# Optimization experiments

Hardware: AMD Instinct MI355X
Metric: run time of the kernel (lower is better)

## Reference

```python
import jax, jax.numpy as jnp
import numpy as np

N_NODES = 50000
N_FEAT = 32
HIDDEN = 64
K_HOPS = 3
N_EDGES = 800000
BN_EPS = 1e-5


def setup_inputs() -> dict:
    key = jax.random.key(0)
    ks = jax.random.split(key, 16)
    x = jax.random.normal(ks[0], (N_NODES, N_FEAT), jnp.float32)
    edge_index = jax.random.randint(ks[1], (2, N_EDGES), 0, N_NODES, jnp.int32)
    edge_weight = jax.random.uniform(ks[2], (N_EDGES,), jnp.float32, minval=0.1, maxval=1.0)
    fin = N_FEAT + HIDDEN  # DCRNN cell concatenates [X, H]
    s = 1.0 / np.sqrt(fin)
    Wz = jax.random.uniform(ks[3], (2, K_HOPS, fin, HIDDEN), jnp.float32, -s, s)
    Wr = jax.random.uniform(ks[4], (2, K_HOPS, fin, HIDDEN), jnp.float32, -s, s)
    Wh = jax.random.uniform(ks[5], (2, K_HOPS, fin, HIDDEN), jnp.float32, -s, s)
    bz = jax.random.uniform(ks[6], (HIDDEN,), jnp.float32, -s, s)
    br = jax.random.uniform(ks[7], (HIDDEN,), jnp.float32, -s, s)
    bh = jax.random.uniform(ks[8], (HIDDEN,), jnp.float32, -s, s)
    g = 1.0 / np.sqrt(HIDDEN)
    gcn_w = jax.random.uniform(ks[9], (HIDDEN, HIDDEN), jnp.float32, -g, g)
    gcn_b = jax.random.uniform(ks[10], (HIDDEN,), jnp.float32, -g, g)
    bn_gamma = jnp.ones((HIDDEN,), jnp.float32)
    bn_beta = jnp.zeros((HIDDEN,), jnp.float32)
    lin_w = jax.random.uniform(ks[11], (HIDDEN, 1), jnp.float32, -g, g)
    lin_b = jax.random.uniform(ks[12], (1,), jnp.float32, -g, g)
    return dict(x=x, edge_index=edge_index, edge_weight=edge_weight,
                Wz=Wz, bz=bz, Wr=Wr, br=br, Wh=Wh, bh=bh,
                gcn_w=gcn_w, gcn_b=gcn_b, bn_gamma=bn_gamma, bn_beta=bn_beta,
                lin_w=lin_w, lin_b=lin_b)


def _dconv(X, W, b, row, col, ew, do_inv, di_inv, n):
    # Diffusion conv: H = sum_k T_out^k(X) @ W[0,k] + T_in^k(X) @ W[1,k] + b
    # T_out: propagate along edges (source -> target), out-degree normalized
    # T_in : propagate along reversed edges, in-degree normalized
    H = X @ W[0, 0] + X @ W[1, 0]
    Tx_o = X
    Tx_i = X
    w_out = (ew * do_inv[row])[:, None]  # [E,1]
    w_in = (ew * di_inv[col])[:, None]   # [E,1]
    for k in range(1, W.shape[1]):
        Tx_o = jax.ops.segment_sum(w_out * Tx_o[row], col, num_segments=n)
        Tx_i = jax.ops.segment_sum(w_in * Tx_i[col], row, num_segments=n)
        H = H + Tx_o @ W[0, k] + Tx_i @ W[1, k]
    return H + b


def reference(x, edge_index, edge_weight, Wz, bz, Wr, br, Wh, bh,
              gcn_w, gcn_b, bn_gamma, bn_beta, lin_w, lin_b):
    n = x.shape[0]
    row, col = edge_index[0], edge_index[1]
    # weighted degrees (as in DConv's dense-adjacency degree computation)
    deg_out = jax.ops.segment_sum(edge_weight, row, num_segments=n)
    deg_in = jax.ops.segment_sum(edge_weight, col, num_segments=n)
    do_inv = jnp.where(deg_out > 0, 1.0 / deg_out, 0.0)
    di_inv = jnp.where(deg_in > 0, 1.0 / deg_in, 0.0)

    # --- DCRNN cell (GRU with diffusion convs), hidden state starts at zero ---
    H0 = jnp.zeros((n, Wz.shape[-1]), x.dtype)
    XH = jnp.concatenate([x, H0], axis=1)
    Z = jax.nn.sigmoid(_dconv(XH, Wz, bz, row, col, edge_weight, do_inv, di_inv, n))
    R = jax.nn.sigmoid(_dconv(XH, Wr, br, row, col, edge_weight, do_inv, di_inv, n))
    XHR = jnp.concatenate([x, H0 * R], axis=1)
    H_tilde = jnp.tanh(_dconv(XHR, Wh, bh, row, col, edge_weight, do_inv, di_inv, n))
    H = Z * H0 + (1.0 - Z) * H_tilde  # [N, HIDDEN]

    # --- GCNConv(H, edge_index) with unit edge weights + self loops, sym norm ---
    xw = H @ gcn_w
    ones_e = jnp.ones((row.shape[0],), x.dtype)
    deg = jax.ops.segment_sum(ones_e, col, num_segments=n) + 1.0  # + self loop
    dis = jnp.where(deg > 0, jax.lax.rsqrt(deg), 0.0)
    norm = (dis[row] * dis[col])[:, None]
    y = jax.ops.segment_sum(norm * xw[row], col, num_segments=n) + (dis * dis)[:, None] * xw
    y = y + gcn_b

    # ReLU -> BatchNorm1d (batch statistics, biased var) -> Dropout(identity/eval) -> Linear
    y = jax.nn.relu(y)
    mean = jnp.mean(y, axis=0)
    var = jnp.mean(jnp.square(y - mean), axis=0)
    y = (y - mean) * jax.lax.rsqrt(var + BN_EPS) * bn_gamma + bn_beta
    out = y @ lin_w + lin_b  # [N, 1]
    return out
```

## Files before the change

### kernel.cpp

```cpp
#include <hip/hip_runtime.h>
#include <hip/hip_fp16.h>
#include <math.h>


#define BN_EPS 1e-5f
#define CAPB 6
#define CAP  64
#define ITEMS 2048
#define KI 8
#define REGCAP 5120

typedef _Float16 v8h __attribute__((ext_vector_type(8)));
typedef float v4f __attribute__((ext_vector_type(4)));

__global__ __launch_bounds__(256) void k_sort1(
    const int* __restrict__ row, const int* __restrict__ col,
    const float* __restrict__ ew,
    unsigned long long* __restrict__ bufC, unsigned long long* __restrict__ bufR,
    unsigned* __restrict__ gcnt, int E, int nbk, int reg) {
    __shared__ unsigned hist[256], scanb[256], cur[256], runb[256];
    __shared__ unsigned long long outb[ITEMS];
    int t = threadIdx.x;
    int s = (blockIdx.x >= nbk) ? 1 : 0;
    int blk = blockIdx.x - s * nbk;
    int e0 = blk * ITEMS;
    int vcnt = E - e0; if (vcnt > ITEMS) vcnt = ITEMS;
    hist[t] = 0;
    __syncthreads();
    for (int k = 0; k < KI; ++k) {
        int e = e0 + k * 256 + t;
        if (e < E) {
            int key = s ? row[e] : col[e];
            atomicAdd(&hist[key >> 8], 1u);
        }
    }
    __syncthreads();
    scanb[t] = hist[t];
    __syncthreads();
    for (int off = 1; off < 256; off <<= 1) {
        unsigned v = (t >= off) ? scanb[t - off] : 0u;
        __syncthreads();
        scanb[t] += v;
        __syncthreads();
    }
    unsigned excl = scanb[t] - hist[t];
    __syncthreads();
    scanb[t] = excl;
    cur[t] = excl;
    runb[t] = (unsigned)(t * reg) + atomicAdd(&gcnt[s * 256 + t], hist[t]);
    __syncthreads();
    for (int k = 0; k < KI; ++k) {
        int e = e0 + k * 256 + t;
        if (e < E) {
            int key, oth;
            if (s) { key = row[e]; oth = col[e]; }
            else   { key = col[e]; oth = row[e]; }
            unsigned hw = (unsigned)__half_as_ushort(__float2half(ew[e]));
            unsigned long long it = ((unsigned long long)(unsigned)key << 32)
                                  | ((unsigned)oth << 16) | hw;
            unsigned r = atomicAdd(&cur[key >> 8], 1u);
            outb[r] = it;
        }
    }
    __syncthreads();
    unsigned long long* buf = s ? bufR : bufC;
    for (int k = 0; k < KI; ++k) {
        int idx = k * 256 + t;
        if (idx < vcnt) {
            unsigned long long it = outb[idx];
            unsigned d = (unsigned)(it >> 40) & 255u;
            buf[(size_t)runb[d] + ((unsigned)idx - scanb[d])] = it;
        }
    }
}

__global__ __launch_bounds__(256) void k_sort2(
    const unsigned long long* __restrict__ buf, const unsigned* __restrict__ gcnt,
    unsigned* __restrict__ ent, int* __restrict__ cnt, int N, int reg) {
    __shared__ unsigned hist[256], scanb[256], cur[256];
    __shared__ unsigned outp[REGCAP];
    __shared__ unsigned char outl[REGCAP];
    int t = threadIdx.x;
    int d0 = blockIdx.x;
    const unsigned long long* src = buf + (size_t)d0 * reg;
    int cin = (int)gcnt[d0]; if (cin > REGCAP) cin = REGCAP;
    hist[t] = 0;
    __syncthreads();
    for (int i = t; i < cin; i += 256) {
        unsigned l = (unsigned)(src[i] >> 32) & 255u;
        atomicAdd(&hist[l], 1u);
    }
    __syncthreads();
    scanb[t] = hist[t];
    __syncthreads();
    for (int off = 1; off < 256; off <<= 1) {
        unsigned v = (t >= off) ? scanb[t - off] : 0u;
        __syncthreads();
        scanb[t] += v;
        __syncthreads();
    }
    unsigned excl = scanb[t] - hist[t];
    __syncthreads();
    scanb[t] = excl;
    cur[t] = excl;
    int node0 = d0 << 8;
    if (node0 + t < N) cnt[node0 + t] = (int)hist[t];
    __syncthreads();
    for (int i = t; i < cin; i += 256) {
        unsigned long long it = src[i];
        unsigned l = (unsigned)(it >> 32) & 255u;
        unsigned r = atomicAdd(&cur[l], 1u);
        outp[r] = (unsigned)it;
        outl[r] = (unsigned char)l;
    }
    __syncthreads();
    for (int i = t; i < cin; i += 256) {
        unsigned l = outl[i];
        int slot = i - (int)scanb[l];
        int node = node0 + (int)l;
        if (slot < CAP && node < N)
            ent[((size_t)node << CAPB) + slot] = outp[i];
    }
}

__device__ inline float ent_w(unsigned e) {
    return __half2float(__ushort_as_half((unsigned short)(e & 0xffffu)));
}

__global__ void k_degs(const unsigned* __restrict__ ent_col, const unsigned* __restrict__ ent_row,
                       const int* __restrict__ cnt_col, const int* __restrict__ cnt_row,
                       float* __restrict__ do_inv, float* __restrict__ di_inv,
                       float* __restrict__ dis, int N) {
    int i = blockIdx.x * blockDim.x + threadIdx.x;
    if (i >= N) return;
    float s = 0.f;
    int c = min(cnt_row[i], CAP);
    const unsigned* er = ent_row + ((size_t)i << CAPB);
    for (int j = 0; j < c; ++j) s += ent_w(er[j]);
    do_inv[i] = s > 0.f ? 1.f / s : 0.f;
    s = 0.f;
    c = min(cnt_col[i], CAP);
    const unsigned* ec = ent_col + ((size_t)i << CAPB);
    for (int j = 0; j < c; ++j) s += ent_w(ec[j]);
    di_inv[i] = s > 0.f ? 1.f / s : 0.f;
    dis[i] = rsqrtf((float)cnt_col[i] + 1.0f);
}

__global__ void k_cvt_x(const float* __restrict__ xf, __half* __restrict__ xh, int n2) {
    int t = blockIdx.x * blockDim.x + threadIdx.x;
    if (t >= n2) return;
    float2 v = *(const float2*)(xf + 2 * (size_t)t);
    __half2 h; h.x = __float2half(v.x); h.y = __float2half(v.y);
    *(__half2*)(xh + 2 * (size_t)t) = h;
}

__global__ void k_hop(const unsigned* __restrict__ ent_col, const unsigned* __restrict__ ent_row,
                      const int* __restrict__ cnt_col, const int* __restrict__ cnt_row,
                      const __half* __restrict__ So, const __half* __restrict__ Si,
                      const float* __restrict__ do_inv, const float* __restrict__ di_inv,
                      __half* __restrict__ Do, __half* __restrict__ Di, int N) {
    int t = blockIdx.x * blockDim.x + threadIdx.x;
    int f = t & 31;
    int p = t >> 5;
    if (p >= 2 * N) return;
    const unsigned* ent; const __half* S; const float* inv; __half* D;
    int d, cnt;
    if (p < N) { d = p;     ent = ent_col; S = So; inv = do_inv; D = Do; cnt = min(cnt_col[d], CAP); }
    else       { d = p - N; ent = ent_row; S = Si; inv = di_inv; D = Di; cnt = min(cnt_row[d], CAP); }
    ent += ((size_t)d << CAPB);
    float acc = 0.f;
    int j = 0;
    for (; j + 7 < cnt; j += 8) {
        unsigned e0 = ent[j],     e1 = ent[j + 1], e2 = ent[j + 2], e3 = ent[j + 3];
        unsigned e4 = ent[j + 4], e5 = ent[j + 5], e6 = ent[j + 6], e7 = ent[j + 7];
        int s0 = e0 >> 16, s1 = e1 >> 16, s2 = e2 >> 16, s3 = e3 >> 16;
        int s4 = e4 >> 16, s5 = e5 >> 16, s6 = e6 >> 16, s7 = e7 >> 16;
        float i0 = inv[s0], i1 = inv[s1], i2 = inv[s2], i3 = inv[s3];
        float i4 = inv[s4], i5 = inv[s5], i6 = inv[s6], i7 = inv[s7];
        float v0 = __half2float(S[(size_t)s0 * 32 + f]);
        float v1 = __half2float(S[(size_t)s1 * 32 + f]);
        float v2 = __half2float(S[(size_t)s2 * 32 + f]);
        float v3 = __half2float(S[(size_t)s3 * 32 + f]);
        float v4 = __half2float(S[(size_t)s4 * 32 + f]);
        float v5 = __half2float(S[(size_t)s5 * 32 + f]);
        float v6 = __half2float(S[(size_t)s6 * 32 + f]);
        float v7 = __half2float(S[(size_t)s7 * 32 + f]);
        acc += ent_w(e0) * i0 * v0 + ent_w(e1) * i1 * v1
             + ent_w(e2) * i2 * v2 + ent_w(e3) * i3 * v3
             + ent_w(e4) * i4 * v4 + ent_w(e5) * i5 * v5
             + ent_w(e6) * i6 * v6 + ent_w(e7) * i7 * v7;
    }
    for (; j + 3 < cnt; j += 4) {
        unsigned e0 = ent[j],     e1 = ent[j + 1];
        unsigned e2 = ent[j + 2], e3 = ent[j + 3];
        int s0 = e0 >> 16, s1 = e1 >> 16, s2 = e2 >> 16, s3 = e3 >> 16;
        float i0 = inv[s0], i1 = inv[s1], i2 = inv[s2], i3 = inv[s3];
        float v0 = __half2float(S[(size_t)s0 * 32 + f]);
        float v1 = __half2float(S[(size_t)s1 * 32 + f]);
        float v2 = __half2float(S[(size_t)s2 * 32 + f]);
        float v3 = __half2float(S[(size_t)s3 * 32 + f]);
        acc += ent_w(e0) * i0 * v0 + ent_w(e1) * i1 * v1
             + ent_w(e2) * i2 * v2 + ent_w(e3) * i3 * v3;
    }
    for (; j < cnt; ++j) {
        unsigned e0 = ent[j];
        int s0 = e0 >> 16;
        acc += ent_w(e0) * inv[s0] * __half2float(S[(size_t)s0 * 32 + f]);
    }
    D[(size_t)d * 32 + f] = __float2half(acc);
}

__global__ void k_wprep(const float* __restrict__ Wz, const float* __restrict__ Wh,
                        const float* __restrict__ gcn_w,
                        __half* __restrict__ wzT, __half* __restrict__ whT,
                        __half* __restrict__ gwT) {
    int t = blockIdx.x * blockDim.x + threadIdx.x;
    if (t < 64 * 160) {
        int c = t / 160, k = t % 160;
        int blk = k >> 5, r = k & 31;
        float vz, vh;
        if (blk == 0) {
            vz = Wz[r * 64 + c] + Wz[(288 + r) * 64 + c];
            vh = Wh[r * 64 + c] + Wh[(288 + r) * 64 + c];
        } else {
            int kk = (blk + 1) >> 1, dd = (blk + 1) & 1;
            int off = ((dd * 3 + kk) * 96 + r) * 64 + c;
            vz = Wz[off]; vh = Wh[off];
        }
        wzT[t] = __float2half(vz);
        whT[t] = __float2half(vh);
    }
    if (t < 64 * 64) {
        int c = t >> 6, k = t & 63;
        gwT[t] = __float2half(gcn_w[k * 64 + c]);
    }
}

__device__ inline v8h ldh8(const __half* p) { return *(const v8h*)p; }

__global__ __launch_bounds__(256) void k_zh_mfma(
    const __half* __restrict__ xh, const __half* __restrict__ t1o,
    const __half* __restrict__ t1i, const __half* __restrict__ t2o,
    const __half* __restrict__ t2i,
    const __half* __restrict__ wzT, const __half* __restrict__ whT,
    const float* __restrict__ bz, const float* __restrict__ bh,
    const float* __restrict__ dis, __half* __restrict__ Hd, int N) {
    int lane = threadIdx.x & 63;
    int wv = threadIdx.x >> 6;
    int q = lane >> 4, m = lane & 15;
    int c = wv * 16 + m;
    int ko = q * 8;

    const __half* wz = wzT + c * 160 + ko;
    const __half* wh = whT + c * 160 + ko;
    v8h bz0 = ldh8(wz),       bh0 = ldh8(wh);
    v8h bz1 = ldh8(wz + 32),  bh1 = ldh8(wh + 32);
    v8h bz2 = ldh8(wz + 64),  bh2 = ldh8(wh + 64);
    v8h bz3 = ldh8(wz + 96),  bh3 = ldh8(wh + 96);
    v8h bz4 = ldh8(wz + 128), bh4 = ldh8(wh + 128);
    float bzc = bz[c], bhc = bh[c];

    int T = (N + 15) >> 4;
    for (int t = blockIdx.x; t < T; t += gridDim.x) {
        int n0 = t << 4;
        int nn = n0 + m; if (nn > N - 1) nn = N - 1;
        size_t off = (size_t)nn * 32 + ko;
        v8h a0 = ldh8(xh + off);
        v8h a1 = ldh8(t1o + off);
        v8h a2 = ldh8(t1i + off);
        v8h a3 = ldh8(t2o + off);
        v8h a4 = ldh8(t2i + off);
        v4f az = {0.f, 0.f, 0.f, 0.f}, ah = {0.f, 0.f, 0.f, 0.f};
        az = __builtin_amdgcn_mfma_f32_16x16x32_f16(a0, bz0, az, 0, 0, 0);
        ah = __builtin_amdgcn_mfma_f32_16x16x32_f16(a0, bh0, ah, 0, 0, 0);
        az = __builtin_amdgcn_mfma_f32_16x16x32_f16(a1, bz1, az, 0, 0, 0);
        ah = __builtin_amdgcn_mfma_f32_16x16x32_f16(a1, bh1, ah, 0, 0, 0);
        az = __builtin_amdgcn_mfma_f32_16x16x32_f16(a2, bz2, az, 0, 0, 0);
        ah = __builtin_amdgcn_mfma_f32_16x16x32_f16(a2, bh2, ah, 0, 0, 0);
        az = __builtin_amdgcn_mfma_f32_16x16x32_f16(a3, bz3, az, 0, 0, 0);
        ah = __builtin_amdgcn_mfma_f32_16x16x32_f16(a3, bh3, ah, 0, 0, 0);
        az = __builtin_amdgcn_mfma_f32_16x16x32_f16(a4, bz4, az, 0, 0, 0);
        ah = __builtin_amdgcn_mfma_f32_16x16x32_f16(a4, bh4, ah, 0, 0, 0);

#pragma unroll
        for (int i = 0; i < 4; ++i) {
            float zv = 1.f / (1.f + expf(-(az[i] + bzc)));
            float hv = (1.f - zv) * tanhf(ah[i] + bhc);
            int node = n0 + q * 4 + i;
            if (node < N) Hd[(size_t)node * 64 + c] = __float2half(dis[node] * hv);
        }
    }
}

__global__ __launch_bounds__(256) void k_agg(
    const unsigned* __restrict__ ent_col, const int* __restrict__ cnt_col,
    const float* __restrict__ dis, const __half* __restrict__ Hd,
    float* __restrict__ P, int N) {
    int t = blockIdx.x * blockDim.x + threadIdx.x;
    int ch = t & 63;
    int d = t >> 6;
    if (d >= N) return;
    const unsigned* ent = ent_col + ((size_t)d << CAPB);
    int cnt = min(cnt_col[d], CAP);
    float acc = __half2float(Hd[(size_t)d * 64 + ch]);
    int j = 0;
    for (; j + 7 < cnt; j += 8) {
        unsigned e0 = ent[j],     e1 = ent[j + 1], e2 = ent[j + 2], e3 = ent[j + 3];
        unsigned e4 = ent[j + 4], e5 = ent[j + 5], e6 = ent[j + 6], e7 = ent[j + 7];
        float v0 = __half2float(Hd[(size_t)(e0 >> 16) * 64 + ch]);
        float v1 = __half2float(Hd[(size_t)(e1 >> 16) * 64 + ch]);
        float v2 = __half2float(Hd[(size_t)(e2 >> 16) * 64 + ch]);
        float v3 = __half2float(Hd[(size_t)(e3 >> 16) * 64 + ch]);
        float v4 = __half2float(Hd[(size_t)(e4 >> 16) * 64 + ch]);
        float v5 = __half2float(Hd[(size_t)(e5 >> 16) * 64 + ch]);
        float v6 = __half2float(Hd[(size_t)(e6 >> 16) * 64 + ch]);
        float v7 = __half2float(Hd[(size_t)(e7 >> 16) * 64 + ch]);
        acc += (v0 + v1 + v2 + v3) + (v4 + v5 + v6 + v7);
    }
    for (; j + 3 < cnt; j += 4) {
        unsigned e0 = ent[j],     e1 = ent[j + 1];
        unsigned e2 = ent[j + 2], e3 = ent[j + 3];
        float v0 = __half2float(Hd[(size_t)(e0 >> 16) * 64 + ch]);
        float v1 = __half2float(Hd[(size_t)(e1 >> 16) * 64 + ch]);
        float v2 = __half2float(Hd[(size_t)(e2 >> 16) * 64 + ch]);
        float v3 = __half2float(Hd[(size_t)(e3 >> 16) * 64 + ch]);
        acc += v0 + v1 + v2 + v3;
    }
    for (; j < cnt; ++j) {
        acc += __half2float(Hd[(size_t)(ent[j] >> 16) * 64 + ch]);
    }
    P[(size_t)d * 64 + ch] = dis[d] * acc;
}

__global__ __launch_bounds__(256) void k_gcn2(
    const float* __restrict__ P, const __half* __restrict__ gwT,
    const float* __restrict__ gcn_b,
    float* __restrict__ y, float* __restrict__ stats, int N) {
    __shared__ float red[2][256];
    int lane = threadIdx.x & 63;
    int wv = threadIdx.x >> 6;
    int q = lane >> 4, m = lane & 15;
    int c = wv * 16 + m;
    int ko = q * 8;
    v8h g0 = ldh8(gwT + c * 64 + ko);
    v8h g1 = ldh8(gwT + c * 64 + 32 + ko);
    float bl = gcn_b[c];
    float sa = 0.f, s2a = 0.f;
    int T = (N + 15) >> 4;
    for (int t = blockIdx.x; t < T; t += gridDim.x) {
        int n0 = t << 4;
        int nn = n0 + m; if (nn > N - 1) nn = N - 1;
        const float* pr = P + (size_t)nn * 64;
        v4f p0 = *(const v4f*)(pr + ko);
        v4f p1 = *(const v4f*)(pr + ko + 4);
        v4f p2 = *(const v4f*)(pr + 32 + ko);
        v4f p3 = *(const v4f*)(pr + 32 + ko + 4);
        v8h a0, a1;
#pragma unroll
        for (int j = 0; j < 4; ++j) {
            a0[j] = (_Float16)p0[j]; a0[4 + j] = (_Float16)p1[j];
            a1[j] = (_Float16)p2[j]; a1[4 + j] = (_Float16)p3[j];
        }
        v4f acc = {0.f, 0.f, 0.f, 0.f};
        acc = __builtin_amdgcn_mfma_f32_16x16x32_f16(a0, g0, acc, 0, 0, 0);
        acc = __builtin_amdgcn_mfma_f32_16x16x32_f16(a1, g1, acc, 0, 0, 0);
#pragma unroll
        for (int i = 0; i < 4; ++i) {
            int node = n0 + q * 4 + i;
            if (node < N) {
                float v = acc[i] + bl;
                v = v > 0.f ? v : 0.f;
                y[(size_t)node * 64 + c] = v;
                sa += v; s2a += v * v;
            }
        }
    }
    red[0][threadIdx.x] = sa;
    red[1][threadIdx.x] = s2a;
    __syncthreads();
    if (q == 0) {
        int t0 = threadIdx.x;
        float ts  = red[0][t0] + red[0][t0 + 16] + red[0][t0 + 32] + red[0][t0 + 48];
        float ts2 = red[1][t0] + red[1][t0 + 16] + red[1][t0 + 32] + red[1][t0 + 48];
        atomicAdd(&stats[c], ts);
        atomicAdd(&stats[64 + c], ts2);
    }
}

__global__ void k_final(const float* __restrict__ y, const float* __restrict__ stats,
                        const float* __restrict__ gma, const float* __restrict__ bta,
                        const float* __restrict__ lw, const float* __restrict__ lb,
                        float* __restrict__ out, int N) {
    int lane = threadIdx.x & 63;
    int wave = (blockIdx.x * blockDim.x + threadIdx.x) >> 6;
    if (wave >= N) return;
    float invN = 1.0f / (float)N;
    float mean = stats[lane] * invN;
    float var  = stats[64 + lane] * invN - mean * mean;
    float istd = rsqrtf(var + BN_EPS);
    float v = y[(size_t)wave * 64 + lane];
    float t = (v - mean) * istd * gma[lane] + bta[lane];
    float p = t * lw[lane];
    for (int off = 32; off > 0; off >>= 1)
        p += __shfl_down(p, off, 64);
    if (lane == 0) out[wave] = p + lb[0];
}

extern "C" void kernel_launch(void* const* d_in, const int* in_sizes, int n_in,
                              void* d_out, int out_size, void* d_ws, size_t ws_size,
                              hipStream_t stream) {
    const float* x     = (const float*)d_in[0];
    const int*   ei    = (const int*)d_in[1];
    const float* ew    = (const float*)d_in[2];
    const float* Wz    = (const float*)d_in[3];
    const float* bz    = (const float*)d_in[4];
    const float* Wh    = (const float*)d_in[7];
    const float* bhv   = (const float*)d_in[8];
    const float* gcn_w = (const float*)d_in[9];
    const float* gcn_b = (const float*)d_in[10];
    const float* gma   = (const float*)d_in[11];
    const float* bta   = (const float*)d_in[12];
    const float* lw    = (const float*)d_in[13];
    const float* lb    = (const float*)d_in[14];
    float* out = (float*)d_out;

    const int N = in_sizes[0] / 32;
    const int E = in_sizes[2];
    const int* row = ei;
    const int* col = ei + E;

    float* ws      = (float*)d_ws;
    int*   cnt_col = (int*)ws;
    int*   cnt_row = (int*)(ws + (size_t)N);
    unsigned* gcnt = (unsigned*)(ws + 2 * (size_t)N);
    float* stats   = ws + 2 * (size_t)N + 512;
    size_t Z0      = 2 * (size_t)N + 640;
    float* dis     = ws + Z0;
    float* do_inv  = ws + Z0 + (size_t)N;
    float* di_inv  = ws + Z0 + 2 * (size_t)N;
    __half* xh     = (__half*)(ws + Z0 + 3 * (size_t)N);
    __half* txo1   = (__half*)(ws + Z0 + 19 * (size_t)N);
    __half* txi1   = (__half*)(ws + Z0 + 35 * (size_t)N);
    __half* txo2   = (__half*)(ws + Z0 + 51 * (size_t)N);
    __half* txi2   = (__half*)(ws + Z0 + 67 * (size_t)N);
    unsigned* ent_col = (unsigned*)(ws + Z0 + 83 * (size_t)N);
    unsigned* ent_row = ent_col + ((size_t)N << CAPB);
    __half* wzT    = (__half*)(ws + Z0 + 211 * (size_t)N);
    __half* whT    = wzT + 64 * 160;
    __half* gwT    = whT + 64 * 160;

    unsigned long long* bufC = (unsigned long long*)ent_row;
    unsigned long long* bufR = (unsigned long long*)txo1;
    __half* Hd = (__half*)ent_row;
    float*  P  = (float*)xh;
    float*  yb = (float*)ent_col;

    size_t zero_bytes = (2 * (size_t)N + 640) * sizeof(float);
    hipMemsetAsync(d_ws, 0, zero_bytes, stream);

    int NB = (N + 255) / 256;
    int nbk = (E + ITEMS - 1) / ITEMS;
    int ndig = (N + 255) / 256;
    k_cvt_x<<<(16 * N + 255) / 256, 256, 0, stream>>>(x, xh, 16 * N);
    k_wprep<<<40, 256, 0, stream>>>(Wz, Wh, gcn_w, wzT, whT, gwT);
    k_sort1<<<2 * nbk, 256, 0, stream>>>(row, col, ew, bufC, bufR, gcnt, E, nbk, REGCAP);
    k_sort2<<<ndig, 256, 0, stream>>>(bufC, gcnt,       ent_col, cnt_col, N, REGCAP);
    k_sort2<<<ndig, 256, 0, stream>>>(bufR, gcnt + 256, ent_row, cnt_row, N, REGCAP);
    k_degs <<<NB, 256, 0, stream>>>(ent_col, ent_row, cnt_col, cnt_row,
                                    do_inv, di_inv, dis, N);

    int bhop = (2 * N * 32 + 255) / 256;
    k_hop<<<bhop, 256, 0, stream>>>(ent_col, ent_row, cnt_col, cnt_row,
                                    xh, xh, do_inv, di_inv, txo1, txi1, N);
    k_hop<<<bhop, 256, 0, stream>>>(ent_col, ent_row, cnt_col, cnt_row,
                                    txo1, txi1, do_inv, di_inv, txo2, txi2, N);

    k_zh_mfma<<<1024, 256, 0, stream>>>(xh, txo1, txi1, txo2, txi2,
                                        wzT, whT, bz, bhv, dis, Hd, N);

    k_agg<<<(64 * N + 255) / 256, 256, 0, stream>>>(ent_col, cnt_col, dis, Hd, P, N);
    k_gcn2<<<1024, 256, 0, stream>>>(P, gwT, gcn_b, yb, stats, N);
    k_final<<<(N + 3) / 4, 256, 0, stream>>>(yb, stats, gma, bta, lw, lb, out, N);
}
```

Before: 298.2 us.

## Fuse degree computation into merged sort2 launch and store GCN intermediate in fp16

```diff
diff --git a/kernel.cpp b/kernel.cpp
--- a/kernel.cpp
+++ b/kernel.cpp
@@ -74,16 +74,26 @@
     }
 }
 
+__device__ inline float ent_w(unsigned e) {
+    return __half2float(__ushort_as_half((unsigned short)(e & 0xffffu)));
+}
+
 __global__ __launch_bounds__(256) void k_sort2(
-    const unsigned long long* __restrict__ buf, const unsigned* __restrict__ gcnt,
-    unsigned* __restrict__ ent, int* __restrict__ cnt, int N, int reg) {
+    const unsigned long long* __restrict__ bufC, const unsigned long long* __restrict__ bufR,
+    const unsigned* __restrict__ gcnt,
+    unsigned* __restrict__ ent_col, unsigned* __restrict__ ent_row,
+    int* __restrict__ cnt_col, int* __restrict__ cnt_row,
+    float* __restrict__ di_inv, float* __restrict__ do_inv, float* __restrict__ dis,
+    int N, int reg, int ndig) {
     __shared__ unsigned hist[256], scanb[256], cur[256];
     __shared__ unsigned outp[REGCAP];
     __shared__ unsigned char outl[REGCAP];
     int t = threadIdx.x;
-    int d0 = blockIdx.x;
-    const unsigned long long* src = buf + (size_t)d0 * reg;
-    int cin = (int)gcnt[d0]; if (cin > REGCAP) cin = REGCAP;
+    int s = (blockIdx.x >= ndig) ? 1 : 0;
+    int d0 = blockIdx.x - s * ndig;
+    const unsigned long long* src = (s ? bufR : bufC) + (size_t)d0 * reg;
+    unsigned* ent = s ? ent_row : ent_col;
+    int cin = (int)gcnt[s * 256 + d0]; if (cin > REGCAP) cin = REGCAP;
     hist[t] = 0;
     __syncthreads();
     for (int i = t; i < cin; i += 256) {
@@ -103,8 +113,6 @@
     __syncthreads();
     scanb[t] = excl;
     cur[t] = excl;
-    int node0 = d0 << 8;
-    if (node0 + t < N) cnt[node0 + t] = (int)hist[t];
     __syncthreads();
     for (int i = t; i < cin; i += 256) {
         unsigned long long it = src[i];
@@ -114,6 +122,7 @@
         outl[r] = (unsigned char)l;
     }
     __syncthreads();
+    int node0 = d0 << 8;
     for (int i = t; i < cin; i += 256) {
         unsigned l = outl[i];
         int slot = i - (int)scanb[l];
@@ -121,29 +130,16 @@
         if (slot < CAP && node < N)
             ent[((size_t)node << CAPB) + slot] = outp[i];
     }
-}
-
-__device__ inline float ent_w(unsigned e) {
-    return __half2float(__ushort_as_half((unsigned short)(e & 0xffffu)));
-}
-
-__global__ void k_degs(const unsigned* __restrict__ ent_col, const unsigned* __restrict__ ent_row,
-                       const int* __restrict__ cnt_col, const int* __restrict__ cnt_row,
-                       float* __restrict__ do_inv, float* __restrict__ di_inv,
-                       float* __restrict__ dis, int N) {
-    int i = blockIdx.x * blockDim.x + threadIdx.x;
-    if (i >= N) return;
-    float s = 0.f;
-    int c = min(cnt_row[i], CAP);
-    const unsigned* er = ent_row + ((size_t)i << CAPB);
-    for (int j = 0; j < c; ++j) s += ent_w(er[j]);
-    do_inv[i] = s > 0.f ? 1.f / s : 0.f;
-    s = 0.f;
-    c = min(cnt_col[i], CAP);
-    const unsigned* ec = ent_col + ((size_t)i << CAPB);
-    for (int j = 0; j < c; ++j) s += ent_w(ec[j]);
-    di_inv[i] = s > 0.f ? 1.f / s : 0.f;
-    dis[i] = rsqrtf((float)cnt_col[i] + 1.0f);
+    int node = node0 + t;
+    if (node < N) {
+        unsigned beg = scanb[t], n = hist[t];
+        float sum = 0.f;
+        for (unsigned j = 0; j < n; ++j) sum += ent_w(outp[beg + j]);
+        float inv = sum > 0.f ? 1.f / sum : 0.f;
+        if (s) { do_inv[node] = inv; cnt_row[node] = (int)n; }
+        else   { di_inv[node] = inv; cnt_col[node] = (int)n;
+                 dis[node] = rsqrtf((float)n + 1.0f); }
+    }
 }
 
 __global__ void k_cvt_x(const float* __restrict__ xf, __half* __restrict__ xh, int n2) {
@@ -295,7 +291,7 @@
 __global__ __launch_bounds__(256) void k_agg(
     const unsigned* __restrict__ ent_col, const int* __restrict__ cnt_col,
     const float* __restrict__ dis, const __half* __restrict__ Hd,
-    float* __restrict__ P, int N) {
+    __half* __restrict__ P, int N) {
     int t = blockIdx.x * blockDim.x + threadIdx.x;
     int ch = t & 63;
     int d = t >> 6;
@@ -329,11 +325,11 @@
     for (; j < cnt; ++j) {
         acc += __half2float(Hd[(size_t)(ent[j] >> 16) * 64 + ch]);
     }
-    P[(size_t)d * 64 + ch] = dis[d] * acc;
+    P[(size_t)d * 64 + ch] = __float2half(dis[d] * acc);
 }
 
 __global__ __launch_bounds__(256) void k_gcn2(
-    const float* __restrict__ P, const __half* __restrict__ gwT,
+    const __half* __restrict__ P, const __half* __restrict__ gwT,
     const float* __restrict__ gcn_b,
     float* __restrict__ y, float* __restrict__ stats, int N) {
     __shared__ float red[2][256];
@@ -350,17 +346,9 @@
     for (int t = blockIdx.x; t < T; t += gridDim.x) {
         int n0 = t << 4;
         int nn = n0 + m; if (nn > N - 1) nn = N - 1;
-        const float* pr = P + (size_t)nn * 64;
-        v4f p0 = *(const v4f*)(pr + ko);
-        v4f p1 = *(const v4f*)(pr + ko + 4);
-        v4f p2 = *(const v4f*)(pr + 32 + ko);
-        v4f p3 = *(const v4f*)(pr + 32 + ko + 4);
-        v8h a0, a1;
-#pragma unroll
-        for (int j = 0; j < 4; ++j) {
-            a0[j] = (_Float16)p0[j]; a0[4 + j] = (_Float16)p1[j];
-            a1[j] = (_Float16)p2[j]; a1[4 + j] = (_Float16)p3[j];
-        }
+        const __half* pr = P + (size_t)nn * 64;
+        v8h a0 = ldh8(pr + ko);
+        v8h a1 = ldh8(pr + 32 + ko);
         v4f acc = {0.f, 0.f, 0.f, 0.f};
         acc = __builtin_amdgcn_mfma_f32_16x16x32_f16(a0, g0, acc, 0, 0, 0);
         acc = __builtin_amdgcn_mfma_f32_16x16x32_f16(a1, g1, acc, 0, 0, 0);
@@ -448,26 +436,24 @@
     __half* wzT    = (__half*)(ws + Z0 + 211 * (size_t)N);
     __half* whT    = wzT + 64 * 160;
     __half* gwT    = whT + 64 * 160;
-
-    unsigned long long* bufC = (unsigned long long*)ent_row;
-    unsigned long long* bufR = (unsigned long long*)txo1;
+    unsigned long long* bufC = (unsigned long long*)(ws + Z0 + 211 * (size_t)N + 16384);
+    unsigned long long* bufR = bufC + (size_t)256 * REGCAP;
+
     __half* Hd = (__half*)ent_row;
-    float*  P  = (float*)xh;
+    __half* P  = (__half*)xh;
     float*  yb = (float*)ent_col;
 
-    size_t zero_bytes = (2 * (size_t)N + 640) * sizeof(float);
-    hipMemsetAsync(d_ws, 0, zero_bytes, stream);
-
-    int NB = (N + 255) / 256;
+    hipMemsetAsync((char*)d_ws + 2 * (size_t)N * sizeof(float), 0,
+                   640 * sizeof(float), stream);
+
     int nbk = (E + ITEMS - 1) / ITEMS;
     int ndig = (N + 255) / 256;
     k_cvt_x<<<(16 * N + 255) / 256, 256, 0, stream>>>(x, xh, 16 * N);
     k_wprep<<<40, 256, 0, stream>>>(Wz, Wh, gcn_w, wzT, whT, gwT);
     k_sort1<<<2 * nbk, 256, 0, stream>>>(row, col, ew, bufC, bufR, gcnt, E, nbk, REGCAP);
-    k_sort2<<<ndig, 256, 0, stream>>>(bufC, gcnt,       ent_col, cnt_col, N, REGCAP);
-    k_sort2<<<ndig, 256, 0, stream>>>(bufR, gcnt + 256, ent_row, cnt_row, N, REGCAP);
-    k_degs <<<NB, 256, 0, stream>>>(ent_col, ent_row, cnt_col, cnt_row,
-                                    do_inv, di_inv, dis, N);
+    k_sort2<<<2 * ndig, 256, 0, stream>>>(bufC, bufR, gcnt, ent_col, ent_row,
+                                          cnt_col, cnt_row, di_inv, do_inv, dis,
+                                          N, REGCAP, ndig);
 
     int bhop = (2 * N * 32 + 255) / 256;
     k_hop<<<bhop, 256, 0, stream>>>(ent_col, ent_row, cnt_col, cnt_row,
```

After: 276.3 us. 1.08x faster.
